# Optimization experiments

Measured on AMD Instinct MI355X. Metric: run time of the kernel, lower is better.

The kernel has to match this reference:

```python
import jax, jax.numpy as jnp
import numpy as np

B, S, D = 32, 1024, 1024   # batch, seq_len, d_model
P, F = 4, 4096             # num_phases, d_ff
# Each phase owns a contiguous split of S/P sequence positions (set_splits builds
# a disjoint contiguous partition of the sequence; assert t == seq_length).


def setup_inputs() -> dict:
    key = jax.random.key(0)
    ks = jax.random.split(key, 6)
    x = jax.random.normal(ks[0], (B, S, D), dtype=jnp.float32)
    phases = jax.random.randint(ks[1], (B, S), 0, P, dtype=jnp.int32)
    s1 = 1.0 / np.sqrt(D)
    s2 = 1.0 / np.sqrt(F)
    W1 = jax.random.uniform(ks[2], (P, D, F), jnp.float32, -s1, s1)
    b1 = jax.random.uniform(ks[3], (P, F), jnp.float32, -s1, s1)
    W2 = jax.random.uniform(ks[4], (P, F, D), jnp.float32, -s2, s2)
    b2 = jax.random.uniform(ks[5], (P, D), jnp.float32, -s2, s2)
    return {"x": x, "W1": W1, "b1": b1, "W2": W2, "b2": b2, "phases": phases}


def reference(x, W1, b1, W2, b2, phases):
    # Branched path (phases.ndim > 1): gather each phase's contiguous split,
    # run that phase's FF, scatter back. Since the static phase_mask is a
    # contiguous equal partition, gather/scatter == reshape into [B, P, S/P, D].
    xs = x.reshape(B, P, S // P, D)
    h = jax.nn.relu(jnp.einsum('bpsd,pdf->bpsf', xs, W1) + b1[None, :, None, :])
    y = jnp.einsum('bpsf,pfd->bpsd', h, W2) + b2[None, :, None, :]
    return y.reshape(B, S, D)
```

## Files before the change

kernel.cpp:

```cpp
#include <hip/hip_runtime.h>
#include <hip/hip_bf16.h>
#include <stdint.h>

typedef __bf16 bf16_t;
typedef bf16_t bf16x8 __attribute__((ext_vector_type(8)));
typedef bf16_t bf16x4 __attribute__((ext_vector_type(4)));
typedef float  f32x4  __attribute__((ext_vector_type(4)));

#define AS1(p) ((const __attribute__((address_space(1))) void*)(p))
#define AS3(p) ((__attribute__((address_space(3))) void*)(p))

static constexpr int B_ = 32, S_ = 1024, D_ = 1024, P_ = 4, F_ = 4096;
static constexpr int SPP = S_ / P_;
static constexpr int MP  = B_ * SPP;

__global__ void conv_x_kernel(const float* __restrict__ x, bf16_t* __restrict__ xg) {
  const int64_t n4 = (int64_t)B_ * S_ * D_ / 4;
  for (int64_t i = (int64_t)blockIdx.x * blockDim.x + threadIdx.x; i < n4;
       i += (int64_t)gridDim.x * blockDim.x) {
    int64_t e = i << 2;
    int d = (int)(e & (D_ - 1));
    int s = (int)((e >> 10) & (S_ - 1));
    int b = (int)(e >> 20);
    int p = s >> 8;
    int r = (b << 8) | (s & 255);
    const float4 v = ((const float4*)x)[i];
    bf16x4 o;
    o[0] = (bf16_t)v.x; o[1] = (bf16_t)v.y; o[2] = (bf16_t)v.z; o[3] = (bf16_t)v.w;
    *(bf16x4*)&xg[(((int64_t)p * MP + r) << 10) | d] = o;
  }
}

__global__ void conv_wt_kernel(const float* __restrict__ W, bf16_t* __restrict__ Wt,
                               int K, int N) {
  __shared__ bf16_t tile[32][33];
  const int p = blockIdx.z;
  const float* Wp = W + (int64_t)p * K * N;
  bf16_t* Wtp = Wt + (int64_t)p * K * N;
  const int n0 = blockIdx.x * 32, k0 = blockIdx.y * 32;
  const int tx = threadIdx.x & 31, ty = threadIdx.x >> 5;
  #pragma unroll
  for (int j = 0; j < 4; ++j) {
    int kr = ty + j * 8;
    tile[kr][tx] = (bf16_t)Wp[(int64_t)(k0 + kr) * N + n0 + tx];
  }
  __syncthreads();
  #pragma unroll
  for (int j = 0; j < 4; ++j) {
    int nr = ty + j * 8;
    Wtp[(int64_t)(n0 + nr) * K + k0 + tx] = tile[tx][nr];
  }
}


__device__ __forceinline__ bf16x8 ldsfrag(const char* region, int row, int cb) {
  return *(const bf16x8*)(region + row * 128 + (cb ^ ((row & 7) << 4)));
}

template<int LDK>
__device__ __forceinline__ void stage_half(const bf16_t* gsrc, char* ldsreg, int t) {
  #pragma unroll
  for (int j = 0; j < 2; ++j) {
    const int idx = j * 512 + t;
    const int row = idx >> 3;
    const int cb  = ((idx & 7) << 4) ^ ((row & 7) << 4);
    __builtin_amdgcn_global_load_lds(AS1((const char*)(gsrc + (int64_t)row * LDK) + cb),
                                     AS3(ldsreg + idx * 16), 16, 0, 0);
  }
}

#define MFMA_QUAD(AF, BF, MO, NO) \
  do { _Pragma("unroll") for (int m_ = 0; m_ < 4; ++m_) \
       _Pragma("unroll") for (int n_ = 0; n_ < 2; ++n_) \
       _Pragma("unroll") for (int k_ = 0; k_ < 2; ++k_) \
         acc[(MO) + m_][(NO) + n_] = __builtin_amdgcn_mfma_f32_16x16x32_bf16( \
             AF[m_][k_], BF[n_][k_], acc[(MO) + m_][(NO) + n_], 0, 0, 0); } while (0)

#define READ_A4(DST, REG, MO) \
  do { _Pragma("unroll") for (int m_ = 0; m_ < 4; ++m_) \
       _Pragma("unroll") for (int k_ = 0; k_ < 2; ++k_) \
         DST[m_][k_] = ldsfrag(REG, wm * 128 + ((MO) + m_) * 16 + fr, k_ * 64 + hi * 16); } while (0)

#define READ_B2(DST, REG, NO) \
  do { _Pragma("unroll") for (int n_ = 0; n_ < 2; ++n_) \
       _Pragma("unroll") for (int k_ = 0; k_ < 2; ++k_) \
         DST[n_][k_] = ldsfrag(REG, wn * 64 + ((NO) + n_) * 16 + fr, k_ * 64 + hi * 16); } while (0)

#define BAR()   __builtin_amdgcn_s_barrier()
#define SBAR()  __builtin_amdgcn_sched_barrier(0)
#define PRIO(x) __builtin_amdgcn_s_setprio(x)
#define VMCNT6() asm volatile("s_waitcnt vmcnt(6)" ::: "memory")
#define VMCNT0() asm volatile("s_waitcnt vmcnt(0)" ::: "memory")
#define LGKM0() do { asm volatile("s_waitcnt lgkmcnt(0)" ::: "memory"); SBAR(); } while (0)
#define LGKM8() asm volatile("s_waitcnt lgkmcnt(8)" ::: "memory")

template<bool RELU, bool OUT_BF16, int KK, int NN>
__global__ __launch_bounds__(512, 2)
void ffgemm8_kernel(const bf16_t* __restrict__ A, const bf16_t* __restrict__ Bt,
                    const float* __restrict__ bias, void* __restrict__ outv, int M) {
  static_assert(KK % 128 == 0, "need even number of 64-wide K tiles");
  __shared__ __align__(16) char smem[131072];
  char* const At0 = smem;
  char* const At1 = smem + 32768;
  char* const Bs0 = smem + 65536;
  char* const Bs1 = smem + 98304;

  const int t = threadIdx.x, lane = t & 63, w = t >> 6;
  const int wm = w >> 2, wn = w & 3;
  const int fr = lane & 15, hi = lane >> 4;

  const int gx = gridDim.x, gy = gridDim.y;
  const int nwg = gx * gy * (int)gridDim.z;
  const int id  = ((int)blockIdx.z * gy + (int)blockIdx.y) * gx + (int)blockIdx.x;
  const int swz = (id & 7) * (nwg >> 3) + (id >> 3);
  const int per_p = gx * gy;
  const int p  = swz / per_p;
  const int q  = swz % per_p;
  const int band = q / (gx * 4), qq = q % (gx * 4);
  const int bx = qq >> 2, by = band * 4 + (qq & 3);

  const int tile_m = by * 256, tile_n = bx * 256;
  const bf16_t* Ab = A  + (int64_t)p * M  * KK + (int64_t)tile_m * KK;
  const bf16_t* Bb = Bt + (int64_t)p * NN * KK + (int64_t)tile_n * KK;
  const float* biasp = bias + (int64_t)p * NN;

  f32x4 acc[8][4] = {};
  constexpr int NI = KK / 128;

  stage_half<KK>(Ab,                          At0,          t);
  stage_half<KK>(Ab + (int64_t)128 * KK,      At0 + 16384,  t);
  stage_half<KK>(Bb,                          Bs0,          t);
  stage_half<KK>(Bb + (int64_t)128 * KK,      Bs0 + 16384,  t);
  stage_half<KK>(Bb + 64,                     Bs1,          t);
  stage_half<KK>(Bb + (int64_t)128 * KK + 64, Bs1 + 16384,  t);
  stage_half<KK>(Ab + 64,                     At1,          t);
  VMCNT6();
  BAR(); SBAR();

  for (int i = 0; i < NI; ++i) {
    const int k0 = i * 128;
    const bool more = (i < NI - 1);
    bf16x8 a0[4][2], a1[4][2], b0[2][2], b1[2][2];

    READ_A4(a0, At0, 0); READ_B2(b0, Bs0, 0);
    stage_half<KK>(Ab + (int64_t)128 * KK + (k0 + 64), At1 + 16384, t);
    LGKM8(); BAR(); LGKM0(); PRIO(1); MFMA_QUAD(a0, b0, 0, 0); PRIO(0); BAR();
    READ_B2(b1, Bs0, 2);
    BAR(); LGKM0(); PRIO(1); MFMA_QUAD(a0, b1, 0, 2); PRIO(0); BAR();
    READ_A4(a1, At0, 4);
    if (more) { stage_half<KK>(Bb + (k0 + 128), Bs0, t);
                stage_half<KK>(Bb + (int64_t)128 * KK + (k0 + 128), Bs0 + 16384, t); }
    BAR(); LGKM0(); PRIO(1); MFMA_QUAD(a1, b0, 4, 0); PRIO(0); BAR();
    if (more) stage_half<KK>(Ab + (k0 + 128), At0, t);
    BAR(); LGKM0(); PRIO(1); MFMA_QUAD(a1, b1, 4, 2); PRIO(0);
    if (more) VMCNT6(); else VMCNT0();
    BAR(); SBAR();

    READ_A4(a0, At1, 0); READ_B2(b0, Bs1, 0);
    if (more) stage_half<KK>(Ab + (int64_t)128 * KK + (k0 + 128), At0 + 16384, t);
    LGKM8(); BAR(); LGKM0(); PRIO(1); MFMA_QUAD(a0, b0, 0, 0); PRIO(0); BAR();
    READ_B2(b1, Bs1, 2);
    BAR(); LGKM0(); PRIO(1); MFMA_QUAD(a0, b1, 0, 2); PRIO(0); BAR();
    READ_A4(a1, At1, 4);
    if (more) { stage_half<KK>(Bb + (k0 + 192), Bs1, t);
                stage_half<KK>(Bb + (int64_t)128 * KK + (k0 + 192), Bs1 + 16384, t); }
    BAR(); LGKM0(); PRIO(1); MFMA_QUAD(a1, b0, 4, 0); PRIO(0); BAR();
    if (more) stage_half<KK>(Ab + (k0 + 192), At1, t);
    BAR(); LGKM0(); PRIO(1); MFMA_QUAD(a1, b1, 4, 2); PRIO(0);
    if (more) VMCNT6(); else VMCNT0();
    BAR(); SBAR();
  }

  float bv[4];
  #pragma unroll
  for (int n = 0; n < 4; ++n) bv[n] = biasp[tile_n + wn * 64 + n * 16 + fr];
  if (OUT_BF16) {
    bf16_t* out = (bf16_t*)outv + (int64_t)p * M * NN;
    #pragma unroll
    for (int m = 0; m < 8; ++m)
      #pragma unroll
      for (int j = 0; j < 4; ++j) {
        const int row = tile_m + wm * 128 + m * 16 + hi * 4 + j;
        #pragma unroll
        for (int n = 0; n < 4; ++n) {
          const int col = tile_n + wn * 64 + n * 16 + fr;
          float v = acc[m][n][j] + bv[n];
          if (RELU) v = fmaxf(v, 0.0f);
          out[(int64_t)row * NN + col] = (bf16_t)v;
        }
      }
  } else {
    float* out = (float*)outv;
    #pragma unroll
    for (int m = 0; m < 8; ++m)
      #pragma unroll
      for (int j = 0; j < 4; ++j) {
        const int row = tile_m + wm * 128 + m * 16 + hi * 4 + j;
        const int grow = ((row >> 8) << 10) + p * SPP + (row & 255);
        #pragma unroll
        for (int n = 0; n < 4; ++n) {
          const int col = tile_n + wn * 64 + n * 16 + fr;
          out[(int64_t)grow * NN + col] = acc[m][n][j] + bv[n];
        }
      }
  }
}

extern "C" void kernel_launch(void* const* d_in, const int* in_sizes, int n_in,
                              void* d_out, int out_size, void* d_ws, size_t ws_size,
                              hipStream_t stream) {
  (void)in_sizes; (void)n_in; (void)out_size; (void)ws_size;
  const float* x  = (const float*)d_in[0];
  const float* W1 = (const float*)d_in[1];
  const float* b1 = (const float*)d_in[2];
  const float* W2 = (const float*)d_in[3];
  const float* b2 = (const float*)d_in[4];
  float* y = (float*)d_out;

  char* ws = (char*)d_ws;
  bf16_t* xg = (bf16_t*)ws;
  bf16_t* wt = (bf16_t*)(ws + (size_t)64 * 1024 * 1024);
  bf16_t* h  = (bf16_t*)(ws + (size_t)96 * 1024 * 1024);

  conv_x_kernel<<<2048, 256, 0, stream>>>(x, xg);
  conv_wt_kernel<<<dim3(F_ / 32, D_ / 32, P_), 256, 0, stream>>>(W1, wt, D_, F_);
  ffgemm8_kernel<true, true, 1024, 4096><<<dim3(F_ / 256, MP / 256, P_), 512, 0, stream>>>(
      xg, wt, b1, h, MP);
  conv_wt_kernel<<<dim3(D_ / 32, F_ / 32, P_), 256, 0, stream>>>(W2, wt, F_, D_);
  ffgemm8_kernel<false, false, 4096, 1024><<<dim3(D_ / 256, MP / 256, P_), 512, 0, stream>>>(
      h, wt, b2, y, MP);
}
```

Before: 575.1 us.

## Hoist all LDS fragment reads per half-tile and cut barriers between MFMA quads

```diff
diff --git a/kernel.cpp b/kernel.cpp
--- a/kernel.cpp
+++ b/kernel.cpp
@@ -91,8 +91,6 @@
 #define PRIO(x) __builtin_amdgcn_s_setprio(x)
 #define VMCNT6() asm volatile("s_waitcnt vmcnt(6)" ::: "memory")
 #define VMCNT0() asm volatile("s_waitcnt vmcnt(0)" ::: "memory")
-#define LGKM0() do { asm volatile("s_waitcnt lgkmcnt(0)" ::: "memory"); SBAR(); } while (0)
-#define LGKM8() asm volatile("s_waitcnt lgkmcnt(8)" ::: "memory")
 
 template<bool RELU, bool OUT_BF16, int KK, int NN>
 __global__ __launch_bounds__(512, 2)
@@ -142,31 +140,31 @@
     const bool more = (i < NI - 1);
     bf16x8 a0[4][2], a1[4][2], b0[2][2], b1[2][2];
 
-    READ_A4(a0, At0, 0); READ_B2(b0, Bs0, 0);
+    READ_A4(a0, At0, 0); READ_B2(b0, Bs0, 0); READ_B2(b1, Bs0, 2); READ_A4(a1, At0, 4);
+    SBAR();
     stage_half<KK>(Ab + (int64_t)128 * KK + (k0 + 64), At1 + 16384, t);
-    LGKM8(); BAR(); LGKM0(); PRIO(1); MFMA_QUAD(a0, b0, 0, 0); PRIO(0); BAR();
-    READ_B2(b1, Bs0, 2);
-    BAR(); LGKM0(); PRIO(1); MFMA_QUAD(a0, b1, 0, 2); PRIO(0); BAR();
-    READ_A4(a1, At0, 4);
+    PRIO(1); MFMA_QUAD(a0, b0, 0, 0); MFMA_QUAD(a0, b1, 0, 2); PRIO(0);
+    BAR(); SBAR();
     if (more) { stage_half<KK>(Bb + (k0 + 128), Bs0, t);
                 stage_half<KK>(Bb + (int64_t)128 * KK + (k0 + 128), Bs0 + 16384, t); }
-    BAR(); LGKM0(); PRIO(1); MFMA_QUAD(a1, b0, 4, 0); PRIO(0); BAR();
+    PRIO(1); MFMA_QUAD(a1, b0, 4, 0); PRIO(0);
+    BAR(); SBAR();
     if (more) stage_half<KK>(Ab + (k0 + 128), At0, t);
-    BAR(); LGKM0(); PRIO(1); MFMA_QUAD(a1, b1, 4, 2); PRIO(0);
+    PRIO(1); MFMA_QUAD(a1, b1, 4, 2); PRIO(0);
     if (more) VMCNT6(); else VMCNT0();
     BAR(); SBAR();
 
-    READ_A4(a0, At1, 0); READ_B2(b0, Bs1, 0);
+    READ_A4(a0, At1, 0); READ_B2(b0, Bs1, 0); READ_B2(b1, Bs1, 2); READ_A4(a1, At1, 4);
+    SBAR();
     if (more) stage_half<KK>(Ab + (int64_t)128 * KK + (k0 + 128), At0 + 16384, t);
-    LGKM8(); BAR(); LGKM0(); PRIO(1); MFMA_QUAD(a0, b0, 0, 0); PRIO(0); BAR();
-    READ_B2(b1, Bs1, 2);
-    BAR(); LGKM0(); PRIO(1); MFMA_QUAD(a0, b1, 0, 2); PRIO(0); BAR();
-    READ_A4(a1, At1, 4);
+    PRIO(1); MFMA_QUAD(a0, b0, 0, 0); MFMA_QUAD(a0, b1, 0, 2); PRIO(0);
+    BAR(); SBAR();
     if (more) { stage_half<KK>(Bb + (k0 + 192), Bs1, t);
                 stage_half<KK>(Bb + (int64_t)128 * KK + (k0 + 192), Bs1 + 16384, t); }
-    BAR(); LGKM0(); PRIO(1); MFMA_QUAD(a1, b0, 4, 0); PRIO(0); BAR();
+    PRIO(1); MFMA_QUAD(a1, b0, 4, 0); PRIO(0);
+    BAR(); SBAR();
     if (more) stage_half<KK>(Ab + (k0 + 192), At1, t);
-    BAR(); LGKM0(); PRIO(1); MFMA_QUAD(a1, b1, 4, 2); PRIO(0);
+    PRIO(1); MFMA_QUAD(a1, b1, 4, 2); PRIO(0);
     if (more) VMCNT6(); else VMCNT0();
     BAR(); SBAR();
   }
```

New measurement: 643.1 us. +11.8%, slower.
